# Optimization experiments

Measured on AMD Instinct MI355X. Metric: run time of the kernel, lower is better.

## Reference

```python
import jax, jax.numpy as jnp
import numpy as np

N_QUBITS = 12
N_LAYERS = 3


def _apply_1q(state, U, q):
    # state: (2,)*N_QUBITS complex64, U: (2,2) single-qubit gate on wire q
    r = jnp.tensordot(U, state, axes=([1], [q]))
    return jnp.moveaxis(r, 0, q)


def _apply_cnot(state, c, t):
    M = jnp.array([[1, 0, 0, 0], [0, 1, 0, 0], [0, 0, 0, 1], [0, 0, 1, 0]],
                  jnp.complex64).reshape(2, 2, 2, 2)
    r = jnp.tensordot(M, state, axes=([2, 3], [c, t]))
    return jnp.moveaxis(r, (0, 1), (c, t))


def circuit_expvals(weights):
    # weights: (N_LAYERS, N_QUBITS, 3). Circuit starts from |0...0> (the
    # TorchLayer 'inputs' arg is a dummy and unused in the original qnode).
    state = jnp.zeros((2,) * N_QUBITS, jnp.complex64).at[(0,) * N_QUBITS].set(1.0)
    zero = jnp.zeros((), jnp.complex64)
    for l in range(N_LAYERS):
        for q in range(N_QUBITS):
            tx, ty, tz = weights[l, q, 0], weights[l, q, 1], weights[l, q, 2]
            cx = jnp.cos(tx / 2).astype(jnp.complex64)
            sx = jnp.sin(tx / 2).astype(jnp.complex64)
            RX = jnp.stack([jnp.stack([cx, -1j * sx]), jnp.stack([-1j * sx, cx])])
            cy = jnp.cos(ty / 2).astype(jnp.complex64)
            sy = jnp.sin(ty / 2).astype(jnp.complex64)
            RY = jnp.stack([jnp.stack([cy, -sy]), jnp.stack([sy, cy])])
            tzc = tz.astype(jnp.complex64)
            em, ep = jnp.exp(-1j * tzc / 2), jnp.exp(1j * tzc / 2)
            RZ = jnp.stack([jnp.stack([em, zero]), jnp.stack([zero, ep])])
            # RX then RY then RZ applied to the state => matrix RZ @ RY @ RX
            state = _apply_1q(state, RZ @ RY @ RX, q)
        for q in range(N_QUBITS):
            state = _apply_cnot(state, q, (q + 1) % N_QUBITS)
    probs = state.real ** 2 + state.imag ** 2
    exps = []
    for q in range(N_QUBITS):
        marg = probs.sum(axis=tuple(a for a in range(N_QUBITS) if a != q))  # (2,)
        exps.append(marg[0] - marg[1])  # <Z_q>
    return jnp.stack(exps).astype(jnp.float32)  # (12,)


def setup_inputs() -> dict:
    key = jax.random.key(0)
    ks = jax.random.split(key, 5)
    B = 1048576
    images = jax.random.uniform(ks[0], (B, 1, 4, 4), dtype=jnp.float32)
    qweights = jax.random.normal(ks[1], (N_LAYERS, N_QUBITS, 3), dtype=jnp.float32)
    W1 = jax.random.normal(ks[2], (32, 12), dtype=jnp.float32) * (1.0 / np.sqrt(12))
    b1 = jnp.zeros((32,), jnp.float32)
    W2 = jax.random.normal(ks[3], (16, 32), dtype=jnp.float32) * (1.0 / np.sqrt(32))
    b2 = jnp.zeros((16,), jnp.float32)
    return {"images": images, "qweights": qweights, "W1": W1, "b1": b1,
            "W2": W2, "b2": b2}


def reference(images, qweights, W1, b1, W2, b2):
    # The original forward ignores the amplitude-encoded image state and runs
    # the identical circuit (dummy zero input) for every batch element, so the
    # per-sample result is constant across the batch.
    z = circuit_expvals(qweights)                     # (12,)
    h = jax.nn.relu(z @ W1.T + b1)                    # (32,)
    pix = jax.nn.sigmoid(h @ W2.T + b2)               # (16,)
    B = images.shape[0]
    return jnp.broadcast_to(pix.reshape(1, 1, 4, 4), (B, 1, 4, 4))
```

## Files before the change

kernel.cpp:

```cpp
#include <hip/hip_runtime.h>
#include <math.h>

#define NTH 512

__device__ __forceinline__ int Sw(int i) { return i ^ ((i >> 6) & 7); }

__device__ __forceinline__ int Fr(int i) {
    int x = i; x ^= x >> 1; x ^= x >> 2; x ^= x >> 4; x ^= x >> 8;
    return (x & 0x7FF) | (((x ^ (i >> 11)) & 1) << 11);
}

__device__ __forceinline__ float2 cmul(float2 a, float2 b) {
    return make_float2(a.x*b.x - a.y*b.y, a.x*b.y + a.y*b.x);
}

__device__ __forceinline__ void apply2(const float4 u0, const float4 u1,
                                       float2& v0, float2& v1) {
    const float n0r = u0.x*v0.x - u0.y*v0.y + u0.z*v1.x - u0.w*v1.y;
    const float n0i = u0.x*v0.y + u0.y*v0.x + u0.z*v1.y + u0.w*v1.x;
    const float n1r = u1.x*v0.x - u1.y*v0.y + u1.z*v1.x - u1.w*v1.y;
    const float n1i = u1.x*v0.y + u1.y*v0.x + u1.z*v1.y + u1.w*v1.x;
    v0 = make_float2(n0r, n0i);
    v1 = make_float2(n1r, n1i);
}

template<int PLOW, int MODE>
__device__ __forceinline__ void do_pass(float2* amp, const float4 (*gmat)[2],
                                        int gbase, int t, float* zacc) {
    int base;
    if      (PLOW == 9) base = t;
    else if (PLOW == 6) base = ((t >> 6) << 9) | (t & 63);
    else if (PLOW == 3) base = ((t >> 3) << 6) | (t & 7);
    else                base = t << 3;

    float2 v[8]; int idx[8];
    #pragma unroll
    for (int r = 0; r < 8; ++r) {
        idx[r] = Sw(base | (r << PLOW));
        v[r] = amp[idx[r]];
    }
    #pragma unroll
    for (int k = 2; k >= 0; --k) {
        const int q = 11 - (PLOW + k);
        const float4 u0 = gmat[gbase + q][0];
        const float4 u1 = gmat[gbase + q][1];
        const int m = 1 << k;
        #pragma unroll
        for (int r = 0; r < 8; ++r)
            if (!(r & m)) apply2(u0, u1, v[r], v[r | m]);
    }
    if (MODE == 0) {
        #pragma unroll
        for (int r = 0; r < 8; ++r) amp[idx[r]] = v[r];
    } else if (MODE == 1) {
        __syncthreads();
        #pragma unroll
        for (int r = 0; r < 8; ++r) amp[Sw(Fr(base | (r << PLOW)))] = v[r];
    } else {
        #pragma unroll
        for (int r = 0; r < 8; ++r) {
            const int x = Fr(base | (r << PLOW));
            const float p = v[r].x*v[r].x + v[r].y*v[r].y;
            #pragma unroll
            for (int q = 0; q < 12; ++q)
                zacc[q] += ((x >> (11 - q)) & 1) ? -p : p;
        }
    }
}

__global__ __launch_bounds__(NTH) void circuit_kernel(
    const float* __restrict__ qw,
    const float* __restrict__ W1,
    const float* __restrict__ b1,
    const float* __restrict__ W2,
    const float* __restrict__ b2,
    float* __restrict__ pix)
{
    __shared__ float2 amp[4096];
    __shared__ float4 gmat[36][2];
    __shared__ float  zp2[96];
    __shared__ float  szv[12];
    __shared__ float  sh[32];

    const int tid = threadIdx.x;

    if (tid < 36) {
        float sx, cx, sy, cy, sz, cz;
        sincosf(0.5f * qw[tid*3+0], &sx, &cx);
        sincosf(0.5f * qw[tid*3+1], &sy, &cy);
        sincosf(0.5f * qw[tid*3+2], &sz, &cz);
        const float a00r =  cy*cx, a00i =  sy*sx;
        const float a01r = -sy*cx, a01i = -cy*sx;
        const float a10r =  sy*cx, a10i = -cy*sx;
        const float a11r =  cy*cx, a11i = -sy*sx;
        gmat[tid][0] = make_float4(cz*a00r + sz*a00i, cz*a00i - sz*a00r,
                                   cz*a01r + sz*a01i, cz*a01i - sz*a01r);
        gmat[tid][1] = make_float4(cz*a10r - sz*a10i, cz*a10i + sz*a10r,
                                   cz*a11r - sz*a11i, cz*a11i + sz*a11r);
    }
    __syncthreads();

    {
        float2 pp = make_float2(1.f, 0.f);
        #pragma unroll
        for (int b = 11; b >= 3; --b) {
            const int q = 11 - b;
            const float4 g = gmat[q][(tid >> (b - 3)) & 1];
            pp = cmul(pp, make_float2(g.x, g.y));
        }
        float2 c9[2], c10[2], c11[2];
        #pragma unroll
        for (int s = 0; s < 2; ++s) {
            c9[s]  = make_float2(gmat[9][s].x,  gmat[9][s].y);
            c10[s] = make_float2(gmat[10][s].x, gmat[10][s].y);
            c11[s] = make_float2(gmat[11][s].x, gmat[11][s].y);
        }
        #pragma unroll
        for (int r = 0; r < 8; ++r) {
            const float2 v = cmul(pp,
                cmul(c9[(r>>2)&1], cmul(c10[(r>>1)&1], c11[r&1])));
            amp[Sw(Fr((tid << 3) | r))] = v;
        }
    }
    __syncthreads();

    float zacc[12];
    #pragma unroll
    for (int q = 0; q < 12; ++q) zacc[q] = 0.f;

    do_pass<9,0>(amp, gmat, 12, tid, zacc); __syncthreads();
    do_pass<6,0>(amp, gmat, 12, tid, zacc); __syncthreads();
    do_pass<3,0>(amp, gmat, 12, tid, zacc); __syncthreads();
    do_pass<0,1>(amp, gmat, 12, tid, zacc); __syncthreads();
    do_pass<9,0>(amp, gmat, 24, tid, zacc); __syncthreads();
    do_pass<6,0>(amp, gmat, 24, tid, zacc); __syncthreads();
    do_pass<3,0>(amp, gmat, 24, tid, zacc); __syncthreads();
    do_pass<0,2>(amp, gmat, 24, tid, zacc);

    const int lane = tid & 63;
    float z6[6];
    #pragma unroll
    for (int k = 0; k < 6; ++k) {
        const float send = (lane & 1) ? zacc[k]     : zacc[k+6];
        const float keep = (lane & 1) ? zacc[k+6]   : zacc[k];
        z6[k] = keep + __shfl_xor(send, 1);
    }
    float z3[3];
    #pragma unroll
    for (int k = 0; k < 3; ++k) {
        const float send = (lane & 2) ? z6[k]   : z6[k+3];
        const float keep = (lane & 2) ? z6[k+3] : z6[k];
        z3[k] = keep + __shfl_xor(send, 2);
    }
    #pragma unroll
    for (int m = 4; m <= 32; m <<= 1) {
        #pragma unroll
        for (int k = 0; k < 3; ++k) z3[k] += __shfl_xor(z3[k], m);
    }
    if (lane < 4) {
        const int qb = 6*(lane & 1) + 3*((lane >> 1) & 1);
        const int w  = tid >> 6;
        #pragma unroll
        for (int k = 0; k < 3; ++k) zp2[w*12 + qb + k] = z3[k];
    }
    __syncthreads();
    if (tid < 12) {
        float s = 0.f;
        #pragma unroll
        for (int w = 0; w < 8; ++w) s += zp2[w*12 + tid];
        szv[tid] = s;
    }
    __syncthreads();

    if (tid < 32) {
        float acc = b1[tid];
        #pragma unroll
        for (int k = 0; k < 12; ++k) acc += W1[tid*12 + k] * szv[k];
        sh[tid] = acc > 0.f ? acc : 0.f;
    }
    __syncthreads();
    if (tid < 16) {
        float acc = b2[tid];
        #pragma unroll
        for (int k = 0; k < 32; ++k) acc += W2[tid*32 + k] * sh[k];
        pix[tid] = 1.f / (1.f + expf(-acc));
    }
}

__global__ __launch_bounds__(256) void bcast_kernel(
    const float4* __restrict__ pix4, float4* __restrict__ out4)
{
    const int i = blockIdx.x * 256 + threadIdx.x;
    out4[i] = pix4[i & 3];
}

extern "C" void kernel_launch(void* const* d_in, const int* in_sizes, int n_in,
                              void* d_out, int out_size, void* d_ws, size_t ws_size,
                              hipStream_t stream) {
    const float* qw = (const float*)d_in[1];
    const float* W1 = (const float*)d_in[2];
    const float* b1 = (const float*)d_in[3];
    const float* W2 = (const float*)d_in[4];
    const float* b2 = (const float*)d_in[5];
    float* pix = (float*)d_ws;

    circuit_kernel<<<1, NTH, 0, stream>>>(qw, W1, b1, W2, b2, pix);

    const int n4 = out_size / 4;
    bcast_kernel<<<n4 / 256, 256, 0, stream>>>((const float4*)pix,
                                               (float4*)d_out);
}
```

Baseline: 123.3 us.

## Use wave shuffles for gates, cut LDS passes, prefetch MLP weights, nontemporal broadcast

Restructures the state-vector simulation so six qubits per layer are applied via cross-lane shuffles and three via registers. This reduces the shared-memory passes and barriers from eight to four. The MLP weights are now prefetched into registers at kernel start, and the MLP reduction uses wave shuffles instead of shared memory and extra barriers. The broadcast kernel now writes its 64 MB output with nontemporal stores, which may help bandwidth but could also hurt it.

Result: slower. 128.0 us (+3.8%).

```diff
diff --git a/kernel.cpp b/kernel.cpp
--- a/kernel.cpp
+++ b/kernel.cpp
@@ -2,6 +2,8 @@
 #include <math.h>
 
 #define NTH 512
+
+typedef float v4f __attribute__((ext_vector_type(4)));
 
 __device__ __forceinline__ int Sw(int i) { return i ^ ((i >> 6) & 7); }
 
@@ -24,47 +26,28 @@
     v1 = make_float2(n1r, n1i);
 }
 
-template<int PLOW, int MODE>
-__device__ __forceinline__ void do_pass(float2* amp, const float4 (*gmat)[2],
-                                        int gbase, int t, float* zacc) {
-    int base;
-    if      (PLOW == 9) base = t;
-    else if (PLOW == 6) base = ((t >> 6) << 9) | (t & 63);
-    else if (PLOW == 3) base = ((t >> 3) << 6) | (t & 7);
-    else                base = t << 3;
-
-    float2 v[8]; int idx[8];
+template<int K>
+__device__ __forceinline__ void reg_gate(float2 v[8], const float4 u0,
+                                         const float4 u1) {
+    #pragma unroll
+    for (int r = 0; r < 8; ++r)
+        if (!(r & (1 << K))) apply2(u0, u1, v[r], v[r | (1 << K)]);
+}
+
+template<int LB>
+__device__ __forceinline__ void lane_gate(float2 v[8], const float4 u0,
+                                          const float4 u1, const int lane) {
+    const int mybit = (lane >> LB) & 1;
+    const float4 rw = mybit ? u1 : u0;
     #pragma unroll
     for (int r = 0; r < 8; ++r) {
-        idx[r] = Sw(base | (r << PLOW));
-        v[r] = amp[idx[r]];
-    }
-    #pragma unroll
-    for (int k = 2; k >= 0; --k) {
-        const int q = 11 - (PLOW + k);
-        const float4 u0 = gmat[gbase + q][0];
-        const float4 u1 = gmat[gbase + q][1];
-        const int m = 1 << k;
-        #pragma unroll
-        for (int r = 0; r < 8; ++r)
-            if (!(r & m)) apply2(u0, u1, v[r], v[r | m]);
-    }
-    if (MODE == 0) {
-        #pragma unroll
-        for (int r = 0; r < 8; ++r) amp[idx[r]] = v[r];
-    } else if (MODE == 1) {
-        __syncthreads();
-        #pragma unroll
-        for (int r = 0; r < 8; ++r) amp[Sw(Fr(base | (r << PLOW)))] = v[r];
-    } else {
-        #pragma unroll
-        for (int r = 0; r < 8; ++r) {
-            const int x = Fr(base | (r << PLOW));
-            const float p = v[r].x*v[r].x + v[r].y*v[r].y;
-            #pragma unroll
-            for (int q = 0; q < 12; ++q)
-                zacc[q] += ((x >> (11 - q)) & 1) ? -p : p;
-        }
+        float2 p;
+        p.x = __shfl_xor(v[r].x, 1 << LB);
+        p.y = __shfl_xor(v[r].y, 1 << LB);
+        const float2 vc = mybit ? p : v[r];
+        const float2 vs = mybit ? v[r] : p;
+        v[r] = make_float2(rw.x*vc.x - rw.y*vc.y + rw.z*vs.x - rw.w*vs.y,
+                           rw.x*vc.y + rw.y*vc.x + rw.z*vs.y + rw.w*vs.x);
     }
 }
 
@@ -79,10 +62,26 @@
     __shared__ float2 amp[4096];
     __shared__ float4 gmat[36][2];
     __shared__ float  zp2[96];
-    __shared__ float  szv[12];
-    __shared__ float  sh[32];
-
-    const int tid = threadIdx.x;
+
+    const int tid  = threadIdx.x;
+    const int lane = tid & 63;
+    const int wv   = tid >> 6;
+
+    float W1row[12], W2row[32], b1v = 0.f, b2v = 0.f;
+    #pragma unroll
+    for (int k = 0; k < 12; ++k) W1row[k] = 0.f;
+    #pragma unroll
+    for (int k = 0; k < 32; ++k) W2row[k] = 0.f;
+    if (tid < 32) {
+        b1v = b1[tid];
+        #pragma unroll
+        for (int k = 0; k < 12; ++k) W1row[k] = W1[tid*12 + k];
+    }
+    if (tid < 16) {
+        b2v = b2[tid];
+        #pragma unroll
+        for (int k = 0; k < 32; ++k) W2row[k] = W2[tid*32 + k];
+    }
 
     if (tid < 36) {
         float sx, cx, sy, cy, sz, cz;
@@ -124,25 +123,80 @@
     }
     __syncthreads();
 
+    float2 v[8];
+
+    {
+        #pragma unroll
+        for (int r = 0; r < 8; ++r) v[r] = amp[Sw((tid << 3) | r)];
+        lane_gate<5>(v, gmat[12+3][0], gmat[12+3][1], lane);
+        lane_gate<4>(v, gmat[12+4][0], gmat[12+4][1], lane);
+        lane_gate<3>(v, gmat[12+5][0], gmat[12+5][1], lane);
+        lane_gate<2>(v, gmat[12+6][0], gmat[12+6][1], lane);
+        lane_gate<1>(v, gmat[12+7][0], gmat[12+7][1], lane);
+        lane_gate<0>(v, gmat[12+8][0], gmat[12+8][1], lane);
+        reg_gate<2>(v, gmat[12+9][0],  gmat[12+9][1]);
+        reg_gate<1>(v, gmat[12+10][0], gmat[12+10][1]);
+        reg_gate<0>(v, gmat[12+11][0], gmat[12+11][1]);
+        #pragma unroll
+        for (int r = 0; r < 8; ++r) amp[Sw((tid << 3) | r)] = v[r];
+    }
+    __syncthreads();
+
+    {
+        #pragma unroll
+        for (int r = 0; r < 8; ++r) v[r] = amp[Sw((r << 9) | (lane << 3) | wv)];
+        reg_gate<2>(v, gmat[12+0][0], gmat[12+0][1]);
+        reg_gate<1>(v, gmat[12+1][0], gmat[12+1][1]);
+        reg_gate<0>(v, gmat[12+2][0], gmat[12+2][1]);
+        __syncthreads();
+        #pragma unroll
+        for (int r = 0; r < 8; ++r)
+            amp[Sw(Fr((r << 9) | (lane << 3) | wv))] = v[r];
+    }
+    __syncthreads();
+
+    {
+        #pragma unroll
+        for (int r = 0; r < 8; ++r) v[r] = amp[Sw((r << 9) | (lane << 3) | wv)];
+        reg_gate<2>(v, gmat[24+0][0], gmat[24+0][1]);
+        reg_gate<1>(v, gmat[24+1][0], gmat[24+1][1]);
+        reg_gate<0>(v, gmat[24+2][0], gmat[24+2][1]);
+        lane_gate<5>(v, gmat[24+3][0], gmat[24+3][1], lane);
+        lane_gate<4>(v, gmat[24+4][0], gmat[24+4][1], lane);
+        lane_gate<3>(v, gmat[24+5][0], gmat[24+5][1], lane);
+        lane_gate<2>(v, gmat[24+6][0], gmat[24+6][1], lane);
+        lane_gate<1>(v, gmat[24+7][0], gmat[24+7][1], lane);
+        lane_gate<0>(v, gmat[24+8][0], gmat[24+8][1], lane);
+        #pragma unroll
+        for (int r = 0; r < 8; ++r)
+            amp[Sw((r << 9) | (lane << 3) | wv)] = v[r];
+    }
+    __syncthreads();
+
     float zacc[12];
     #pragma unroll
     for (int q = 0; q < 12; ++q) zacc[q] = 0.f;
-
-    do_pass<9,0>(amp, gmat, 12, tid, zacc); __syncthreads();
-    do_pass<6,0>(amp, gmat, 12, tid, zacc); __syncthreads();
-    do_pass<3,0>(amp, gmat, 12, tid, zacc); __syncthreads();
-    do_pass<0,1>(amp, gmat, 12, tid, zacc); __syncthreads();
-    do_pass<9,0>(amp, gmat, 24, tid, zacc); __syncthreads();
-    do_pass<6,0>(amp, gmat, 24, tid, zacc); __syncthreads();
-    do_pass<3,0>(amp, gmat, 24, tid, zacc); __syncthreads();
-    do_pass<0,2>(amp, gmat, 24, tid, zacc);
-
-    const int lane = tid & 63;
+    {
+        #pragma unroll
+        for (int r = 0; r < 8; ++r) v[r] = amp[Sw((tid << 3) | r)];
+        reg_gate<2>(v, gmat[24+9][0],  gmat[24+9][1]);
+        reg_gate<1>(v, gmat[24+10][0], gmat[24+10][1]);
+        reg_gate<0>(v, gmat[24+11][0], gmat[24+11][1]);
+        #pragma unroll
+        for (int r = 0; r < 8; ++r) {
+            const int x = Fr((tid << 3) | r);
+            const float p = v[r].x*v[r].x + v[r].y*v[r].y;
+            #pragma unroll
+            for (int q = 0; q < 12; ++q)
+                zacc[q] += ((x >> (11 - q)) & 1) ? -p : p;
+        }
+    }
+
     float z6[6];
     #pragma unroll
     for (int k = 0; k < 6; ++k) {
-        const float send = (lane & 1) ? zacc[k]     : zacc[k+6];
-        const float keep = (lane & 1) ? zacc[k+6]   : zacc[k];
+        const float send = (lane & 1) ? zacc[k]   : zacc[k+6];
+        const float keep = (lane & 1) ? zacc[k+6] : zacc[k];
         z6[k] = keep + __shfl_xor(send, 1);
     }
     float z3[3];
@@ -159,39 +213,34 @@
     }
     if (lane < 4) {
         const int qb = 6*(lane & 1) + 3*((lane >> 1) & 1);
-        const int w  = tid >> 6;
-        #pragma unroll
-        for (int k = 0; k < 3; ++k) zp2[w*12 + qb + k] = z3[k];
-    }
-    __syncthreads();
-    if (tid < 12) {
+        #pragma unroll
+        for (int k = 0; k < 3; ++k) zp2[wv*12 + qb + k] = z3[k];
+    }
+    __syncthreads();
+
+    if (tid < 64) {
         float s = 0.f;
-        #pragma unroll
-        for (int w = 0; w < 8; ++w) s += zp2[w*12 + tid];
-        szv[tid] = s;
-    }
-    __syncthreads();
-
-    if (tid < 32) {
-        float acc = b1[tid];
-        #pragma unroll
-        for (int k = 0; k < 12; ++k) acc += W1[tid*12 + k] * szv[k];
-        sh[tid] = acc > 0.f ? acc : 0.f;
-    }
-    __syncthreads();
-    if (tid < 16) {
-        float acc = b2[tid];
-        #pragma unroll
-        for (int k = 0; k < 32; ++k) acc += W2[tid*32 + k] * sh[k];
-        pix[tid] = 1.f / (1.f + expf(-acc));
+        if (tid < 12) {
+            #pragma unroll
+            for (int w8 = 0; w8 < 8; ++w8) s += zp2[w8*12 + tid];
+        }
+        float acc = b1v;
+        #pragma unroll
+        for (int k = 0; k < 12; ++k) acc += W1row[k] * __shfl(s, k);
+        const float h = acc > 0.f ? acc : 0.f;
+        float acc2 = b2v;
+        #pragma unroll
+        for (int k = 0; k < 32; ++k) acc2 += W2row[k] * __shfl(h, k);
+        if (tid < 16) pix[tid] = 1.f / (1.f + expf(-acc2));
     }
 }
 
 __global__ __launch_bounds__(256) void bcast_kernel(
-    const float4* __restrict__ pix4, float4* __restrict__ out4)
+    const v4f* __restrict__ pix4, v4f* __restrict__ out4)
 {
     const int i = blockIdx.x * 256 + threadIdx.x;
-    out4[i] = pix4[i & 3];
+    const v4f val = pix4[i & 3];
+    __builtin_nontemporal_store(val, &out4[i]);
 }
 
 extern "C" void kernel_launch(void* const* d_in, const int* in_sizes, int n_in,
@@ -207,6 +256,6 @@
     circuit_kernel<<<1, NTH, 0, stream>>>(qw, W1, b1, W2, b2, pix);
 
     const int n4 = out_size / 4;
-    bcast_kernel<<<n4 / 256, 256, 0, stream>>>((const float4*)pix,
-                                               (float4*)d_out);
-}
+    bcast_kernel<<<n4 / 256, 256, 0, stream>>>((const v4f*)pix,
+                                               (v4f*)d_out);
+}
```
